# Kernel tuning notes

Hardware: AMD Instinct MI355X
Metric: run time of the kernel (lower is better)

Reference implementation:

```python
import jax, jax.numpy as jnp
import numpy as np
from jax import lax

B, N, CIN, MID, OUT, G, H, CHILDS = 16, 1024, 256, 512, 256, 4, 1, 512


def _ln(x, g, b, eps=1e-6):
    m = x.mean(-1, keepdims=True)
    v = ((x - m) ** 2).mean(-1, keepdims=True)
    return (x - m) / jnp.sqrt(v + eps) * g + b


def _gconv(x, W, b):
    # grouped 1x1 conv1d: x [B,Cin,N], W [Cout, Cin//G], b [Cout]
    Bb, Cin, Nn = x.shape
    Cout = W.shape[0]
    xg = x.reshape(Bb, G, Cin // G, Nn)
    Wg = W.reshape(G, Cout // G, Cin // G)
    y = jnp.einsum('bgcn,goc->bgon', xg, Wg).reshape(Bb, Cout, Nn)
    return y + b[None, :, None]


def _forward(x, masks_roi1, masks_roi2, score_mask, gt_feat,
             W_att, b_att, W1, b1, W2, b2, g1, beta1, g2, beta2, Wg, bg):
    dt = x.dtype
    # gt branch
    gts = jax.nn.relu(gt_feat @ Wg + bg)  # [B,N,OUT]

    mr1 = masks_roi1 * score_mask[:, None, :]
    mr2 = masks_roi2 * score_mask[:, None, :]

    # attention logits without materializing the [B,N,N,2C] concat:
    # ft[b,i,j] = cat(x[b,j], x[b,i]);  logits = ft @ W_att + b_att
    Wq, Wk = W_att[:CIN], W_att[CIN:]
    lj = jnp.einsum('bjc,ch->bjh', x, Wq)  # query part (varies over j)
    li = jnp.einsum('bic,ch->bih', x, Wk)  # key part   (varies over i)
    attn = jax.nn.sigmoid(lj[:, None, :, :] + li[:, :, None, :] + b_att)  # [B,N,N,H]

    attn1 = attn * mr1[:, :, :, None]
    attn2 = attn * mr2[:, :, :, None]

    # torch fancy-index assign atten_mask[:,:,idces,:]=1 reduces to: any column
    # index appearing in ANY topk index set gets 1 along dim 2 for all b,i,h.
    k4, k2 = CHILDS // 4, CHILDS // 2
    a1 = jnp.moveaxis(attn1, 2, 3)  # [B,N,H,N] -> topk over last axis (= dim 2)
    a2 = jnp.moveaxis(attn2, 2, 3)
    idx1 = lax.top_k(a1, k4)[1]
    idx1m = lax.top_k(-a1, k4)[1]
    idx2 = lax.top_k(a2, k2)[1]
    idx2m = lax.top_k(-a2, k4)[1]
    all_idx = jnp.concatenate([idx1.ravel(), idx1m.ravel(), idx2.ravel(), idx2m.ravel()])
    col = jnp.zeros((N,), dtype=dt).at[all_idx].set(1.0)

    attn = attn * (mr1 + mr2)[:, :, :, None] * col[None, None, :, None]

    f = (score_mask == 0).astype(dt)  # [B,N]
    f_diag = f[:, :, None] * jnp.eye(N, dtype=dt)  # diag_embed
    atten = (attn + f_diag[:, :, :, None]) / CHILDS
    atten = jnp.transpose(atten, (0, 3, 2, 1))  # [B,H,Nj,Ni]

    x_t = jnp.transpose(x, (0, 2, 1))  # [B,CIN,N]
    o1 = jax.nn.relu(_gconv(x_t, W1, b1))  # [B,MID,N]
    o1m = jnp.matmul(o1.reshape(B, H, MID // H, N), atten).reshape(B, MID, N)
    o1m = _ln(jnp.transpose(o1m, (0, 2, 1)), g1, beta1)  # [B,N,MID]
    o1 = o1 + jnp.transpose(o1m, (0, 2, 1))

    o2 = jax.nn.relu(_gconv(o1, W2, b2))  # [B,OUT,N]
    o2m = jnp.matmul(o2.reshape(B, H, OUT // H, N), atten).reshape(B, OUT, N)
    node_feat = _ln(jnp.transpose(o2m, (0, 2, 1)), g2, beta2)  # [B,N,OUT]
    o2 = o2 + jnp.transpose(node_feat, (0, 2, 1))
    output2 = jnp.transpose(o2, (0, 2, 1))  # [B,N,OUT]
    return output2, gts, node_feat


def setup_inputs() -> dict:
    key = jax.random.key(0)
    ks = jax.random.split(key, 16)
    x = jax.random.normal(ks[0], (B, N, CIN), jnp.float32)
    masks_roi1 = (jax.random.uniform(ks[1], (B, N, N)) < 0.1).astype(jnp.float32)
    masks_roi2 = (jax.random.uniform(ks[2], (B, N, N)) < 0.1).astype(jnp.float32)
    score_mask = (jax.random.uniform(ks[3], (B, N)) < 0.8).astype(jnp.float32)
    gt_feat = jax.random.normal(ks[4], (B, N, CIN), jnp.float32)
    s = 0.05
    W_att = jax.random.normal(ks[5], (2 * CIN, H), jnp.float32) * s
    b_att = jnp.zeros((H,), jnp.float32)
    W1 = jax.random.normal(ks[6], (MID, CIN // G), jnp.float32) * s
    b1 = jax.random.normal(ks[7], (MID,), jnp.float32) * s
    W2 = jax.random.normal(ks[8], (OUT, MID // G), jnp.float32) * s
    b2 = jax.random.normal(ks[9], (OUT,), jnp.float32) * s
    g1 = jax.random.normal(ks[10], (MID,), jnp.float32) * s
    beta1 = jnp.zeros((MID,), jnp.float32)
    g2 = jax.random.normal(ks[11], (OUT,), jnp.float32) * s
    beta2 = jnp.zeros((OUT,), jnp.float32)
    Wg = jax.random.normal(ks[12], (CIN, OUT), jnp.float32) * s
    bg = jax.random.normal(ks[13], (OUT,), jnp.float32) * s
    return {"x": x, "masks_roi1": masks_roi1, "masks_roi2": masks_roi2,
            "score_mask": score_mask, "gt_feat": gt_feat,
            "W_att": W_att, "b_att": b_att, "W1": W1, "b1": b1,
            "W2": W2, "b2": b2, "g1": g1, "beta1": beta1,
            "g2": g2, "beta2": beta2, "Wg": Wg, "bg": bg}


def reference(x, masks_roi1, masks_roi2, score_mask, gt_feat,
              W_att, b_att, W1, b1, W2, b2, g1, beta1, g2, beta2, Wg, bg):
    return _forward(x, masks_roi1, masks_roi2, score_mask, gt_feat,
                    W_att, b_att, W1, b1, W2, b2, g1, beta1, g2, beta2, Wg, bg)
```

## Files before the change

### kernel.cpp

```cpp
#include <hip/hip_runtime.h>
#include <cstddef>
#include <cstdint>

#define B_ 16
#define N_ 1024
#define CIN_ 256
#define MID_ 512
#define OUT_ 256

typedef __attribute__((ext_vector_type(8))) short short8v;
typedef __attribute__((ext_vector_type(4))) float f32x4;

__device__ __forceinline__ float sigf(float z){ return 1.f/(1.f+expf(-z)); }
__device__ __forceinline__ ushort f2bf(float f){
  uint32_t u=__float_as_uint(f);
  uint32_t r=(u + 0x7fffu + ((u>>16)&1u))>>16;
  return (ushort)r;
}
__device__ __forceinline__ float bf2f(ushort u){ return __uint_as_float(((uint32_t)u)<<16); }

__device__ __forceinline__ void async16(void* lds, const void* g){
  __builtin_amdgcn_global_load_lds(
      (const __attribute__((address_space(1))) uint32_t*)g,
      (__attribute__((address_space(3))) uint32_t*)lds,
      16, 0, 0);
}

__global__ __launch_bounds__(256) void k_prep(const float* __restrict__ x,
    const float* __restrict__ Watt, float* __restrict__ lj, float* __restrict__ li)
{
  int bn = blockIdx.x*256 + threadIdx.x;
  const float4* xr = (const float4*)(x + (size_t)bn*CIN_);
  const float4* wq = (const float4*)(Watt);
  const float4* wk = (const float4*)(Watt + CIN_);
  float aq=0.f, ak=0.f;
  #pragma unroll 8
  for(int c=0;c<CIN_/4;++c){
    float4 xv=xr[c]; float4 q=wq[c]; float4 w=wk[c];
    aq += xv.x*q.x+xv.y*q.y+xv.z*q.z+xv.w*q.w;
    ak += xv.x*w.x+xv.y*w.y+xv.z*w.z+xv.w*w.w;
  }
  lj[bn]=aq; li[bn]=ak;
}

__global__ __launch_bounds__(256) void k_cast(const float* __restrict__ s, ushort* __restrict__ d){
  int i = blockIdx.x*256 + threadIdx.x;
  float4 v = ((const float4*)s)[i];
  ((ushort4*)d)[i] = make_ushort4(f2bf(v.x), f2bf(v.y), f2bf(v.z), f2bf(v.w));
}
__global__ __launch_bounds__(256) void k_wgtb(const float* __restrict__ Wg, ushort* __restrict__ WgTb){
  int o=blockIdx.x, c=threadIdx.x;
  WgTb[(size_t)o*CIN_ + c] = f2bf(Wg[(size_t)c*OUT_ + o]);
}

__global__ __launch_bounds__(256) void k_col(
    const float* __restrict__ m1, const float* __restrict__ m2,
    const float* __restrict__ sc, const float* __restrict__ lj,
    const float* __restrict__ li, const float* __restrict__ batt,
    float* __restrict__ colf, ushort* __restrict__ mrs)
{
  int row = blockIdx.x; int b = row >> 10; int t = threadIdx.x;
  size_t base = (size_t)row*N_ + 4*t;
  float4 m1v = *(const float4*)(m1 + base);
  float4 m2v = *(const float4*)(m2 + base);
  float4 scv = *(const float4*)(sc + (b<<10) + 4*t);
  float mr1[4] = {m1v.x*scv.x, m1v.y*scv.y, m1v.z*scv.z, m1v.w*scv.w};
  float mr2[4] = {m2v.x*scv.x, m2v.y*scv.y, m2v.z*scv.z, m2v.w*scv.w};
  *(ushort4*)(mrs + base) = make_ushort4(f2bf(mr1[0]+mr2[0]), f2bf(mr1[1]+mr2[1]),
                                         f2bf(mr1[2]+mr2[2]), f2bf(mr1[3]+mr2[3]));
  int z1=0,z2=0;
  #pragma unroll
  for(int k=0;k<4;++k){ z1 += (mr1[k]==0.f); z2 += (mr2[k]==0.f); }
  __shared__ int sc1[256], sc2[256];
  __shared__ float A1s[1024], A2s[1024];
  sc1[t]=z1; sc2[t]=z2; __syncthreads();
  for(int off=1; off<256; off<<=1){
    int a=0,c=0;
    if(t>=off){ a=sc1[t-off]; c=sc2[t-off]; }
    __syncthreads();
    if(t>=off){ sc1[t]+=a; sc2[t]+=c; }
    __syncthreads();
  }
  int excl1 = sc1[t]-z1, excl2 = sc2[t]-z2;
  int Z1 = sc1[255], Z2 = sc2[255];
  int P1 = 1024-Z1, P2 = 1024-Z2;
  bool rare = (P1>128)||(P2>256)||(Z1<128)||(Z2<128);
  if(!rare){
    int zb1=excl1, zb2=excl2;
    #pragma unroll
    for(int k=0;k<4;++k){
      bool q = (mr1[k]!=0.f) || (zb1<128) || (mr2[k]!=0.f) || (zb2<128) || (P2+zb2<256);
      if(q) colf[4*t+k]=1.0f;
      zb1 += (mr1[k]==0.f); zb2 += (mr2[k]==0.f);
    }
  } else {
    float lir = li[row], ba = batt[0];
    float4 ljv = *(const float4*)(lj + (b<<10) + 4*t);
    float ljr[4]={ljv.x,ljv.y,ljv.z,ljv.w};
    #pragma unroll
    for(int k=0;k<4;++k){
      float v = sigf(ljr[k]+lir+ba);
      A1s[4*t+k]=mr1[k]*v; A2s[4*t+k]=mr2[k]*v;
    }
    __syncthreads();
    for(int k=0;k<4;++k){
      int j=4*t+k; float a1j=A1s[j], a2j=A2s[j];
      int r1=0,r1m=0,r2=0,r2m=0;
      for(int jp=0;jp<1024;++jp){
        float p1=A1s[jp], p2=A2s[jp];
        bool lo = jp<j;
        r1  += (p1>a1j)||((p1==a1j)&&lo);
        r1m += (p1<a1j)||((p1==a1j)&&lo);
        r2  += (p2>a2j)||((p2==a2j)&&lo);
        r2m += (p2<a2j)||((p2==a2j)&&lo);
      }
      if(r1<128||r1m<128||r2<256||r2m<128) colf[j]=1.0f;
    }
  }
}

__global__ __launch_bounds__(256) void k_at(const ushort* __restrict__ mrs,
    const float* __restrict__ sc, const float* __restrict__ lj,
    const float* __restrict__ li, const float* __restrict__ batt,
    const float* __restrict__ colf, ushort* __restrict__ Atb)
{
  int row=blockIdx.x, t=threadIdx.x; int b=row>>10, i=row&1023;
  size_t base=(size_t)row*N_ + 4*t;
  ushort4 mv=*(const ushort4*)(mrs+base);
  float4 ljv=*(const float4*)(lj + (b<<10) + 4*t);
  float4 cv =*(const float4*)(colf + 4*t);
  float lir=li[row], ba=batt[0];
  float fi = (sc[(b<<10)+i]==0.f)?1.f:0.f;
  float mra[4]={bf2f(mv.x),bf2f(mv.y),bf2f(mv.z),bf2f(mv.w)};
  float ljr[4]={ljv.x,ljv.y,ljv.z,ljv.w};
  float cr[4]={cv.x,cv.y,cv.z,cv.w};
  ushort o[4]; int j0=4*t;
  #pragma unroll
  for(int k=0;k<4;++k){
    float v=sigf(ljr[k]+lir+ba);
    float val=v*mra[k]*cr[k];
    if(j0+k==i) val+=fi;
    o[k]=f2bf(val*(1.f/512.f));
  }
  *(ushort4*)(Atb+base) = make_ushort4(o[0],o[1],o[2],o[3]);
}

__global__ __launch_bounds__(256) void mgemm(
    const ushort* __restrict__ A, int lda, long long sAb, long long sAg,
    const ushort* __restrict__ Bp, int ldb, long long sBb, long long sBg,
    float* __restrict__ C, ushort* __restrict__ Cb, int ldc, long long sCb, long long sCg,
    int K, int nG,
    const float* __restrict__ biasM, int biasMG,
    const float* __restrict__ biasN, int relu)
{
  __shared__ __align__(16) ushort As[128*32];
  __shared__ __align__(16) ushort Bs[128*32];
  int z=blockIdx.z, b=z/nG, g=z%nG;
  A  += b*sAb + g*sAg;
  Bp += b*sBb + g*sBg;
  size_t cOff = (size_t)b*sCb + (size_t)g*sCg;
  int m0 = blockIdx.y*128, n0 = blockIdx.x*128;
  int tid=threadIdx.x, w=tid>>6, lane=tid&63;
  int la=lane&15, hi=lane>>4;
  int wr=w>>1, wc=w&1;
  f32x4 acc[4][4] = {};
  int sr = tid>>2;
  int sk = (tid&3)*8;
  char* lA = (char*)As + w*1024;
  char* lB = (char*)Bs + w*1024;
  const ushort* gA0 = A + (size_t)(m0+sr)*lda + sk;
  const ushort* gA1 = A + (size_t)(m0+64+sr)*lda + sk;
  const ushort* gB0 = Bp + (size_t)(n0+sr)*ldb + sk;
  const ushort* gB1 = Bp + (size_t)(n0+64+sr)*ldb + sk;
  for(int k0=0;k0<K;k0+=32){
    async16(lA,        gA0 + k0);
    async16(lA + 4096, gA1 + k0);
    async16(lB,        gB0 + k0);
    async16(lB + 4096, gB1 + k0);
    __syncthreads();
    short8v af[4], bf[4];
    #pragma unroll
    for(int i2=0;i2<4;++i2) af[i2] = *(const short8v*)&As[(wr*64+i2*16+la)*32 + hi*8];
    #pragma unroll
    for(int j2=0;j2<4;++j2) bf[j2] = *(const short8v*)&Bs[(wc*64+j2*16+la)*32 + hi*8];
    #pragma unroll
    for(int i2=0;i2<4;++i2)
      #pragma unroll
      for(int j2=0;j2<4;++j2)
        acc[i2][j2] = __builtin_amdgcn_mfma_f32_16x16x32_bf16(af[i2], bf[j2], acc[i2][j2], 0,0,0);
    __syncthreads();
  }
  float* Cp = C + cOff;
  ushort* Cbp = Cb ? Cb + cOff : (ushort*)0;
  #pragma unroll
  for(int i2=0;i2<4;++i2){
    int row0 = m0 + wr*64 + i2*16 + hi*4;
    #pragma unroll
    for(int j2=0;j2<4;++j2){
      int col = n0 + wc*64 + j2*16 + la;
      float bn = biasN ? biasN[col] : 0.f;
      #pragma unroll
      for(int r=0;r<4;++r){
        int row = row0 + r;
        float v = acc[i2][j2][r] + bn + (biasM ? biasM[(size_t)g*biasMG + row] : 0.f);
        if(relu) v = fmaxf(v, 0.f);
        Cp[(size_t)row*ldc + col] = v;
        if(Cbp) Cbp[(size_t)row*ldc + col] = f2bf(v);
      }
    }
  }
}

template<int BM,int BN,int TM,int TN>
__global__ __launch_bounds__(256) void gemm_nt(
    const float* __restrict__ A, int lda, long long sAb, long long sAg,
    const float* __restrict__ Bp, int ldb, long long sBb, long long sBg,
    float* __restrict__ C, ushort* __restrict__ Cbd, int ldc, long long sCb, long long sCg,
    int K, int nG,
    const float* __restrict__ biasM, int biasMG,
    const float* __restrict__ biasN, int relu)
{
  static_assert(TN==4 && BM/TM==16 && BN/TN==16, "layout");
  constexpr int BK=32, LDSS=BK+4;
  int z=blockIdx.z, b=z/nG, g=z%nG;
  A  += b*sAb + g*sAg;
  Bp += b*sBb + g*sBg;
  size_t cOff = (size_t)b*sCb + (size_t)g*sCg;
  __shared__ float As[BM*LDSS];
  __shared__ float Bs[BN*LDSS];
  int tid=threadIdx.x;
  int tx=tid&15, ty=tid>>4;
  int m0=blockIdx.y*BM, n0=blockIdx.x*BN;
  float acc[TM][TN]={};
  for(int k0=0;k0<K;k0+=BK){
    #pragma unroll
    for(int u=0;u<BM*BK/1024;++u){
      int f=u*256+tid, r=f>>3, c=(f&7)*4;
      *(float4*)&As[r*LDSS+c] = *(const float4*)(A + (size_t)(m0+r)*lda + k0 + c);
    }
    #pragma unroll
    for(int u=0;u<BN*BK/1024;++u){
      int f=u*256+tid, r=f>>3, c=(f&7)*4;
      *(float4*)&Bs[r*LDSS+c] = *(const float4*)(Bp + (size_t)(n0+r)*ldb + k0 + c);
    }
    __syncthreads();
    #pragma unroll
    for(int kk=0;kk<BK;kk+=4){
      float4 av[TM]; float4 bv[TN];
      #pragma unroll
      for(int r=0;r<TM;++r) av[r]=*(const float4*)&As[(ty*TM+r)*LDSS+kk];
      #pragma unroll
      for(int c=0;c<TN;++c) bv[c]=*(const float4*)&Bs[(tx*TN+c)*LDSS+kk];
      #pragma unroll
      for(int r=0;r<TM;++r){
        #pragma unroll
        for(int c=0;c<TN;++c){
          acc[r][c] += av[r].x*bv[c].x + av[r].y*bv[c].y + av[r].z*bv[c].z + av[r].w*bv[c].w;
        }
      }
    }
    __syncthreads();
  }
  float4 bnv=make_float4(0.f,0.f,0.f,0.f);
  if(biasN){ bnv=*(const float4*)(biasN + n0 + tx*TN); }
  #pragma unroll
  for(int r=0;r<TM;++r){
    int m=m0+ty*TM+r;
    float bm = biasM ? biasM[(size_t)g*biasMG + m] : 0.f;
    float4 v;
    v.x=acc[r][0]+bm+bnv.x;
    v.y=acc[r][1]+bm+bnv.y;
    v.z=acc[r][2]+bm+bnv.z;
    v.w=acc[r][3]+bm+bnv.w;
    if(relu){ v.x=fmaxf(v.x,0.f); v.y=fmaxf(v.y,0.f); v.z=fmaxf(v.z,0.f); v.w=fmaxf(v.w,0.f); }
    *(float4*)(C + cOff + (size_t)m*ldc + n0 + tx*TN) = v;
    if(Cbd){
      *(ushort4*)(Cbd + cOff + (size_t)m*ldc + n0 + tx*TN) =
          make_ushort4(f2bf(v.x), f2bf(v.y), f2bf(v.z), f2bf(v.w));
    }
  }
}

__global__ __launch_bounds__(256) void k_ln1(const float* o1mT, const float* o1,
    const float* __restrict__ g1v, const float* __restrict__ be1, float* o1pT)
{
  int row=blockIdx.x, t=threadIdx.x; int b=row>>10, i=row&1023;
  float2 v = ((const float2*)(o1mT + (size_t)row*MID_))[t];
  float s=v.x+v.y, s2=v.x*v.x+v.y*v.y;
  for(int off=32; off; off>>=1){ s+=__shfl_down(s,off); s2+=__shfl_down(s2,off); }
  __shared__ float sm[8];
  int lane=t&63, wid=t>>6;
  if(lane==0){ sm[wid]=s; sm[4+wid]=s2; }
  __syncthreads();
  s=sm[0]+sm[1]+sm[2]+sm[3]; s2=sm[4]+sm[5]+sm[6]+sm[7];
  float mean=s*(1.f/MID_), var=s2*(1.f/MID_)-mean*mean;
  float rstd=rsqrtf(var+1e-6f);
  int m0=2*t;
  float a0=(v.x-mean)*rstd*g1v[m0]+be1[m0];
  float a1=(v.y-mean)*rstd*g1v[m0+1]+be1[m0+1];
  float2 o;
  o.x = a0 + o1[((size_t)(b*MID_+m0  ))*N_ + i];
  o.y = a1 + o1[((size_t)(b*MID_+m0+1))*N_ + i];
  ((float2*)(o1pT + (size_t)row*MID_))[t] = o;
}

__global__ __launch_bounds__(256) void k_ln2f(const float* o2mT, const float* o2,
    const float* __restrict__ g2v, const float* __restrict__ be2,
    float* node, float* out2)
{
  int row=blockIdx.x, t=threadIdx.x; int b=row>>10, i=row&1023;
  float v = o2mT[(size_t)row*OUT_ + t];
  float s=v, s2=v*v;
  for(int off=32; off; off>>=1){ s+=__shfl_down(s,off); s2+=__shfl_down(s2,off); }
  __shared__ float sm[8];
  int lane=t&63, wid=t>>6;
  if(lane==0){ sm[wid]=s; sm[4+wid]=s2; }
  __syncthreads();
  s=sm[0]+sm[1]+sm[2]+sm[3]; s2=sm[4]+sm[5]+sm[6]+sm[7];
  float mean=s*(1.f/OUT_); float var=s2*(1.f/OUT_)-mean*mean;
  float rstd=rsqrtf(var+1e-6f);
  float nf=(v-mean)*rstd*g2v[t]+be2[t];
  size_t ro=(size_t)row*OUT_+t;
  node[ro]=nf;
  out2[ro]=nf + o2[((size_t)(b*OUT_+t))*N_ + i];
}

extern "C" void kernel_launch(void* const* d_in, const int* in_sizes, int n_in,
                              void* d_out, int out_size, void* d_ws, size_t ws_size,
                              hipStream_t stream)
{
  const float* x    = (const float*)d_in[0];
  const float* m1   = (const float*)d_in[1];
  const float* m2   = (const float*)d_in[2];
  const float* sc   = (const float*)d_in[3];
  const float* gt   = (const float*)d_in[4];
  const float* Watt = (const float*)d_in[5];
  const float* batt = (const float*)d_in[6];
  const float* W1   = (const float*)d_in[7];
  const float* b1   = (const float*)d_in[8];
  const float* W2   = (const float*)d_in[9];
  const float* b2   = (const float*)d_in[10];
  const float* g1   = (const float*)d_in[11];
  const float* be1  = (const float*)d_in[12];
  const float* g2   = (const float*)d_in[13];
  const float* be2  = (const float*)d_in[14];
  const float* Wg   = (const float*)d_in[15];
  const float* bg   = (const float*)d_in[16];

  float* out2 = (float*)d_out;
  float* gtso = out2 + (size_t)B_*N_*OUT_;
  float* node = gtso + (size_t)B_*N_*OUT_;

  char* ws = (char*)d_ws;
  float*  colf = (float*)(ws);
  float*  lj   = (float*)(ws + 4096);
  float*  li   = (float*)(ws + 69632);
  ushort* WgTb = (ushort*)(ws + 135168);
  ushort* W1b  = (ushort*)(ws + 266240);
  ushort* gtb  = (ushort*)(ws + 331776);
  ushort* Atb  = (ushort*)(ws + 8720384);
  float*  o1   = (float*)(ws + 42274816);
  ushort* o1b  = (ushort*)(ws + 75829248);
  char*   big32 = ws + 92606464;
  ushort* mrs  = (ushort*)big32;
  ushort* xb   = (ushort*)big32;
  float*  o1mT = (float*)big32;
  float*  o1pT = o1mT;
  float*  o2   = o1;
  ushort* o2b  = o1b;
  float*  o2mT = o1mT;

  hipMemsetAsync(colf, 0, 4096, stream);
  k_prep<<<dim3(B_*N_/256),dim3(256),0,stream>>>(x,Watt,lj,li);
  k_col <<<dim3(B_*N_),dim3(256),0,stream>>>(m1,m2,sc,lj,li,batt,colf,mrs);
  k_at  <<<dim3(B_*N_),dim3(256),0,stream>>>(mrs,sc,lj,li,batt,colf,Atb);

  k_cast<<<dim3(4096),dim3(256),0,stream>>>(x, xb);
  k_cast<<<dim3(4096),dim3(256),0,stream>>>(gt, gtb);
  k_cast<<<dim3(32),dim3(256),0,stream>>>(W1, W1b);
  k_wgtb<<<dim3(OUT_),dim3(256),0,stream>>>(Wg, WgTb);

  mgemm<<<dim3(2,128,1),256,0,stream>>>(
      gtb, CIN_, 0,0,
      WgTb, CIN_, 0,0,
      gtso, (ushort*)0, OUT_, 0,0,
      CIN_, 1, nullptr,0, bg, 1);

  mgemm<<<dim3(8,1,B_*4),256,0,stream>>>(
      W1b, 64, 0, (long long)128*64,
      xb, CIN_, (long long)N_*CIN_, 64,
      o1, o1b, N_, (long long)MID_*N_, (long long)128*N_,
      64, 4, b1, 128, nullptr, 1);

  mgemm<<<dim3(4,8,B_),256,0,stream>>>(
      Atb, N_, (long long)N_*N_, 0,
      o1b, N_, (long long)MID_*N_, 0,
      o1mT, (ushort*)0, MID_, (long long)N_*MID_, 0,
      N_, 1, nullptr,0, nullptr, 0);

  k_ln1<<<dim3(B_*N_),256,0,stream>>>(o1mT, o1, g1, be1, o1pT);

  gemm_nt<64,64,4,4><<<dim3(N_/64, 1, B_*4),256,0,stream>>>(
      W2, 128, 0, (long long)64*128,
      o1pT, MID_, (long long)N_*MID_, 128,
      o2, o2b, N_, (long long)OUT_*N_, (long long)64*N_,
      128, 4, b2, 64, nullptr, 1);

  mgemm<<<dim3(2,8,B_),256,0,stream>>>(
      Atb, N_, (long long)N_*N_, 0,
      o2b, N_, (long long)OUT_*N_, 0,
      o2mT, (ushort*)0, OUT_, (long long)N_*OUT_, 0,
      N_, 1, nullptr,0, nullptr, 0);

  k_ln2f<<<dim3(B_*N_),256,0,stream>>>(o2mT, o2, g2, be2, node, out2);
}
```

Baseline: 468.3 us.

## Move W2 GEMM to bf16 MFMA, drop fp32 intermediates, warp-per-row k_col

Replaces the fp32 SIMT gemm_nt for the W2 grouped conv with a templated bf16 MFMA GEMM, and stops writing fp32 copies of o1/o2 by reading residuals from the bf16 buffers. It also merges the cast kernels into fewer launches and rewrites k_col to process one row per wavefront using shuffle scans instead of block-level LDS scans. The rare fallback path now recomputes values from global memory instead of using shared memory. Residual adds now use bf16-rounded values, which adds precision risk.

```diff
diff --git a/kernel.cpp b/kernel.cpp
--- a/kernel.cpp
+++ b/kernel.cpp
@@ -43,14 +43,23 @@
   lj[bn]=aq; li[bn]=ak;
 }
 
-__global__ __launch_bounds__(256) void k_cast(const float* __restrict__ s, ushort* __restrict__ d){
+__global__ __launch_bounds__(256) void k_cast2(const float* __restrict__ x,
+    const float* __restrict__ gt, ushort* __restrict__ xb, ushort* __restrict__ gtb)
+{
   int i = blockIdx.x*256 + threadIdx.x;
-  float4 v = ((const float4*)s)[i];
-  ((ushort4*)d)[i] = make_ushort4(f2bf(v.x), f2bf(v.y), f2bf(v.z), f2bf(v.w));
-}
-__global__ __launch_bounds__(256) void k_wgtb(const float* __restrict__ Wg, ushort* __restrict__ WgTb){
-  int o=blockIdx.x, c=threadIdx.x;
-  WgTb[(size_t)o*CIN_ + c] = f2bf(Wg[(size_t)c*OUT_ + o]);
+  int which = i>>20; int idx = i & 1048575;
+  float4 v = ((const float4*)(which ? gt : x))[idx];
+  ((ushort4*)(which ? gtb : xb))[idx] = make_ushort4(f2bf(v.x), f2bf(v.y), f2bf(v.z), f2bf(v.w));
+}
+
+__global__ __launch_bounds__(256) void k_wcast(const float* __restrict__ W1,
+    const float* __restrict__ W2, const float* __restrict__ Wg,
+    ushort* __restrict__ W1b, ushort* __restrict__ W2b, ushort* __restrict__ WgTb)
+{
+  int bid=blockIdx.x, t=threadIdx.x;
+  if(bid<128){ int i=bid*256+t; W1b[i]=f2bf(W1[i]); }
+  else if(bid<256){ int i=(bid-128)*256+t; W2b[i]=f2bf(W2[i]); }
+  else { int idx=(bid-256)*256+t; int o=idx>>8, c=idx&255; WgTb[idx]=f2bf(Wg[(size_t)c*OUT_+o]); }
 }
 
 __global__ __launch_bounds__(256) void k_col(
@@ -59,62 +68,71 @@
     const float* __restrict__ li, const float* __restrict__ batt,
     float* __restrict__ colf, ushort* __restrict__ mrs)
 {
-  int row = blockIdx.x; int b = row >> 10; int t = threadIdx.x;
-  size_t base = (size_t)row*N_ + 4*t;
-  float4 m1v = *(const float4*)(m1 + base);
-  float4 m2v = *(const float4*)(m2 + base);
-  float4 scv = *(const float4*)(sc + (b<<10) + 4*t);
-  float mr1[4] = {m1v.x*scv.x, m1v.y*scv.y, m1v.z*scv.z, m1v.w*scv.w};
-  float mr2[4] = {m2v.x*scv.x, m2v.y*scv.y, m2v.z*scv.z, m2v.w*scv.w};
-  *(ushort4*)(mrs + base) = make_ushort4(f2bf(mr1[0]+mr2[0]), f2bf(mr1[1]+mr2[1]),
-                                         f2bf(mr1[2]+mr2[2]), f2bf(mr1[3]+mr2[3]));
-  int z1=0,z2=0;
-  #pragma unroll
-  for(int k=0;k<4;++k){ z1 += (mr1[k]==0.f); z2 += (mr2[k]==0.f); }
-  __shared__ int sc1[256], sc2[256];
-  __shared__ float A1s[1024], A2s[1024];
-  sc1[t]=z1; sc2[t]=z2; __syncthreads();
-  for(int off=1; off<256; off<<=1){
-    int a=0,c=0;
-    if(t>=off){ a=sc1[t-off]; c=sc2[t-off]; }
-    __syncthreads();
-    if(t>=off){ sc1[t]+=a; sc2[t]+=c; }
-    __syncthreads();
-  }
-  int excl1 = sc1[t]-z1, excl2 = sc2[t]-z2;
-  int Z1 = sc1[255], Z2 = sc2[255];
-  int P1 = 1024-Z1, P2 = 1024-Z2;
+  int wid = threadIdx.x>>6, lane = threadIdx.x&63;
+  int row = blockIdx.x*4 + wid; int b = row>>10;
+  size_t base = (size_t)row*N_ + lane*16;
+  const float4* m1p = (const float4*)(m1+base);
+  const float4* m2p = (const float4*)(m2+base);
+  const float4* scp = (const float4*)(sc + (b<<10) + lane*16);
+  float mr1[16], mr2[16];
+  int z1=0, z2=0;
+  #pragma unroll
+  for(int q=0;q<4;++q){
+    float4 a=m1p[q], c=m2p[q], s=scp[q];
+    mr1[4*q+0]=a.x*s.x; mr1[4*q+1]=a.y*s.y; mr1[4*q+2]=a.z*s.z; mr1[4*q+3]=a.w*s.w;
+    mr2[4*q+0]=c.x*s.x; mr2[4*q+1]=c.y*s.y; mr2[4*q+2]=c.z*s.z; mr2[4*q+3]=c.w*s.w;
+    #pragma unroll
+    for(int k=0;k<4;++k){ z1 += (mr1[4*q+k]==0.f); z2 += (mr2[4*q+k]==0.f); }
+  }
+  ushort mb[16];
+  #pragma unroll
+  for(int k=0;k<16;++k) mb[k]=f2bf(mr1[k]+mr2[k]);
+  *(short8v*)(mrs+base)   = *(short8v*)&mb[0];
+  *(short8v*)(mrs+base+8) = *(short8v*)&mb[8];
+  int s1=z1, s2=z2;
+  #pragma unroll
+  for(int off=1; off<64; off<<=1){
+    int t1=__shfl_up(s1,off), t2=__shfl_up(s2,off);
+    if(lane>=off){ s1+=t1; s2+=t2; }
+  }
+  int excl1=s1-z1, excl2=s2-z2;
+  int Z1=__shfl(s1,63), Z2=__shfl(s2,63);
+  int P1=1024-Z1, P2=1024-Z2;
   bool rare = (P1>128)||(P2>256)||(Z1<128)||(Z2<128);
   if(!rare){
     int zb1=excl1, zb2=excl2;
     #pragma unroll
-    for(int k=0;k<4;++k){
+    for(int k=0;k<16;++k){
       bool q = (mr1[k]!=0.f) || (zb1<128) || (mr2[k]!=0.f) || (zb2<128) || (P2+zb2<256);
-      if(q) colf[4*t+k]=1.0f;
+      if(q) colf[lane*16+k]=1.0f;
       zb1 += (mr1[k]==0.f); zb2 += (mr2[k]==0.f);
     }
   } else {
-    float lir = li[row], ba = batt[0];
-    float4 ljv = *(const float4*)(lj + (b<<10) + 4*t);
-    float ljr[4]={ljv.x,ljv.y,ljv.z,ljv.w};
-    #pragma unroll
-    for(int k=0;k<4;++k){
-      float v = sigf(ljr[k]+lir+ba);
-      A1s[4*t+k]=mr1[k]*v; A2s[4*t+k]=mr2[k]*v;
-    }
-    __syncthreads();
-    for(int k=0;k<4;++k){
-      int j=4*t+k; float a1j=A1s[j], a2j=A2s[j];
-      int r1=0,r1m=0,r2=0,r2m=0;
-      for(int jp=0;jp<1024;++jp){
-        float p1=A1s[jp], p2=A2s[jp];
+    float lir=li[row], ba=batt[0];
+    const float* m1r = m1 + (size_t)row*N_;
+    const float* m2r = m2 + (size_t)row*N_;
+    const float* scr = sc + (b<<10);
+    const float* ljr = lj + (b<<10);
+    float a1v[16], a2v[16];
+    #pragma unroll
+    for(int k=0;k<16;++k){
+      float v = sigf(ljr[lane*16+k]+lir+ba);
+      a1v[k]=mr1[k]*v; a2v[k]=mr2[k]*v;
+    }
+    for(int k=0;k<16;++k){
+      int j = lane*16+k;
+      int c1=0,c1m=0,c2=0,c2m=0;
+      for(int jp=0;jp<N_;++jp){
+        float sv=scr[jp];
+        float vv=sigf(ljr[jp]+lir+ba);
+        float p1=m1r[jp]*sv*vv, p2=m2r[jp]*sv*vv;
         bool lo = jp<j;
-        r1  += (p1>a1j)||((p1==a1j)&&lo);
-        r1m += (p1<a1j)||((p1==a1j)&&lo);
-        r2  += (p2>a2j)||((p2==a2j)&&lo);
-        r2m += (p2<a2j)||((p2==a2j)&&lo);
+        c1 += (p1>a1v[k])||((p1==a1v[k])&&lo);
+        c1m+= (p1<a1v[k])||((p1==a1v[k])&&lo);
+        c2 += (p2>a2v[k])||((p2==a2v[k])&&lo);
+        c2m+= (p2<a2v[k])||((p2==a2v[k])&&lo);
       }
-      if(r1<128||r1m<128||r2<256||r2m<128) colf[j]=1.0f;
+      if(c1<128||c1m<128||c2<256||c2m<128) colf[j]=1.0f;
     }
   }
 }
@@ -145,6 +163,7 @@
   *(ushort4*)(Atb+base) = make_ushort4(o[0],o[1],o[2],o[3]);
 }
 
+template<int BM,int BN,int WR,int WC>
 __global__ __launch_bounds__(256) void mgemm(
     const ushort* __restrict__ A, int lda, long long sAb, long long sAg,
     const ushort* __restrict__ Bp, int ldb, long long sBb, long long sBg,
@@ -153,45 +172,46 @@
     const float* __restrict__ biasM, int biasMG,
     const float* __restrict__ biasN, int relu)
 {
-  __shared__ __align__(16) ushort As[128*32];
-  __shared__ __align__(16) ushort Bs[128*32];
+  static_assert(WR*WC==4 && BM==WR*64 && BN==WC*64, "tile");
+  __shared__ __align__(16) ushort As[BM*32];
+  __shared__ __align__(16) ushort Bs[BN*32];
   int z=blockIdx.z, b=z/nG, g=z%nG;
-  A  += b*sAb + g*sAg;
-  Bp += b*sBb + g*sBg;
+  A  += (size_t)b*sAb + (size_t)g*sAg;
+  Bp += (size_t)b*sBb + (size_t)g*sBg;
   size_t cOff = (size_t)b*sCb + (size_t)g*sCg;
-  int m0 = blockIdx.y*128, n0 = blockIdx.x*128;
+  int m0 = blockIdx.y*BM, n0 = blockIdx.x*BN;
   int tid=threadIdx.x, w=tid>>6, lane=tid&63;
   int la=lane&15, hi=lane>>4;
-  int wr=w>>1, wc=w&1;
+  int wr=w/WC, wc=w%WC;
   f32x4 acc[4][4] = {};
-  int sr = tid>>2;
-  int sk = (tid&3)*8;
-  char* lA = (char*)As + w*1024;
-  char* lB = (char*)Bs + w*1024;
-  const ushort* gA0 = A + (size_t)(m0+sr)*lda + sk;
-  const ushort* gA1 = A + (size_t)(m0+64+sr)*lda + sk;
-  const ushort* gB0 = Bp + (size_t)(n0+sr)*ldb + sk;
-  const ushort* gB1 = Bp + (size_t)(n0+64+sr)*ldb + sk;
+  constexpr int RND = (BM+BN)/64;
+  int srow = lane>>2;
+  int sk8  = (lane&3)*8;
   for(int k0=0;k0<K;k0+=32){
-    async16(lA,        gA0 + k0);
-    async16(lA + 4096, gA1 + k0);
-    async16(lB,        gB0 + k0);
-    async16(lB + 4096, gB1 + k0);
+    #pragma unroll
+    for(int r=0;r<RND;++r){
+      int row0 = r*64 + w*16;
+      if(row0 < BM){
+        const ushort* src = A + (size_t)(m0+row0+srow)*lda + k0 + sk8;
+        async16((char*)As + row0*64, src);
+      } else {
+        const ushort* src = Bp + (size_t)(n0+row0-BM+srow)*ldb + k0 + sk8;
+        async16((char*)Bs + (row0-BM)*64, src);
+      }
+    }
     __syncthreads();
-    short8v af[4], bf[4];
+    short8v af[4], bf4[4];
     #pragma unroll
     for(int i2=0;i2<4;++i2) af[i2] = *(const short8v*)&As[(wr*64+i2*16+la)*32 + hi*8];
     #pragma unroll
-    for(int j2=0;j2<4;++j2) bf[j2] = *(const short8v*)&Bs[(wc*64+j2*16+la)*32 + hi*8];
+    for(int j2=0;j2<4;++j2) bf4[j2] = *(const short8v*)&Bs[(wc*64+j2*16+la)*32 + hi*8];
     #pragma unroll
     for(int i2=0;i2<4;++i2)
       #pragma unroll
       for(int j2=0;j2<4;++j2)
-        acc[i2][j2] = __builtin_amdgcn_mfma_f32_16x16x32_bf16(af[i2], bf[j2], acc[i2][j2], 0,0,0);
+        acc[i2][j2] = __builtin_amdgcn_mfma_f32_16x16x32_bf16(af[i2], bf4[j2], acc[i2][j2], 0,0,0);
     __syncthreads();
   }
-  float* Cp = C + cOff;
-  ushort* Cbp = Cb ? Cb + cOff : (ushort*)0;
   #pragma unroll
   for(int i2=0;i2<4;++i2){
     int row0 = m0 + wr*64 + i2*16 + hi*4;
@@ -204,85 +224,16 @@
         int row = row0 + r;
         float v = acc[i2][j2][r] + bn + (biasM ? biasM[(size_t)g*biasMG + row] : 0.f);
         if(relu) v = fmaxf(v, 0.f);
-        Cp[(size_t)row*ldc + col] = v;
-        if(Cbp) Cbp[(size_t)row*ldc + col] = f2bf(v);
+        if(C)  C [cOff + (size_t)row*ldc + col] = v;
+        if(Cb) Cb[cOff + (size_t)row*ldc + col] = f2bf(v);
       }
     }
   }
 }
 
-template<int BM,int BN,int TM,int TN>
-__global__ __launch_bounds__(256) void gemm_nt(
-    const float* __restrict__ A, int lda, long long sAb, long long sAg,
-    const float* __restrict__ Bp, int ldb, long long sBb, long long sBg,
-    float* __restrict__ C, ushort* __restrict__ Cbd, int ldc, long long sCb, long long sCg,
-    int K, int nG,
-    const float* __restrict__ biasM, int biasMG,
-    const float* __restrict__ biasN, int relu)
-{
-  static_assert(TN==4 && BM/TM==16 && BN/TN==16, "layout");
-  constexpr int BK=32, LDSS=BK+4;
-  int z=blockIdx.z, b=z/nG, g=z%nG;
-  A  += b*sAb + g*sAg;
-  Bp += b*sBb + g*sBg;
-  size_t cOff = (size_t)b*sCb + (size_t)g*sCg;
-  __shared__ float As[BM*LDSS];
-  __shared__ float Bs[BN*LDSS];
-  int tid=threadIdx.x;
-  int tx=tid&15, ty=tid>>4;
-  int m0=blockIdx.y*BM, n0=blockIdx.x*BN;
-  float acc[TM][TN]={};
-  for(int k0=0;k0<K;k0+=BK){
-    #pragma unroll
-    for(int u=0;u<BM*BK/1024;++u){
-      int f=u*256+tid, r=f>>3, c=(f&7)*4;
-      *(float4*)&As[r*LDSS+c] = *(const float4*)(A + (size_t)(m0+r)*lda + k0 + c);
-    }
-    #pragma unroll
-    for(int u=0;u<BN*BK/1024;++u){
-      int f=u*256+tid, r=f>>3, c=(f&7)*4;
-      *(float4*)&Bs[r*LDSS+c] = *(const float4*)(Bp + (size_t)(n0+r)*ldb + k0 + c);
-    }
-    __syncthreads();
-    #pragma unroll
-    for(int kk=0;kk<BK;kk+=4){
-      float4 av[TM]; float4 bv[TN];
-      #pragma unroll
-      for(int r=0;r<TM;++r) av[r]=*(const float4*)&As[(ty*TM+r)*LDSS+kk];
-      #pragma unroll
-      for(int c=0;c<TN;++c) bv[c]=*(const float4*)&Bs[(tx*TN+c)*LDSS+kk];
-      #pragma unroll
-      for(int r=0;r<TM;++r){
-        #pragma unroll
-        for(int c=0;c<TN;++c){
-          acc[r][c] += av[r].x*bv[c].x + av[r].y*bv[c].y + av[r].z*bv[c].z + av[r].w*bv[c].w;
-        }
-      }
-    }
-    __syncthreads();
-  }
-  float4 bnv=make_float4(0.f,0.f,0.f,0.f);
-  if(biasN){ bnv=*(const float4*)(biasN + n0 + tx*TN); }
-  #pragma unroll
-  for(int r=0;r<TM;++r){
-    int m=m0+ty*TM+r;
-    float bm = biasM ? biasM[(size_t)g*biasMG + m] : 0.f;
-    float4 v;
-    v.x=acc[r][0]+bm+bnv.x;
-    v.y=acc[r][1]+bm+bnv.y;
-    v.z=acc[r][2]+bm+bnv.z;
-    v.w=acc[r][3]+bm+bnv.w;
-    if(relu){ v.x=fmaxf(v.x,0.f); v.y=fmaxf(v.y,0.f); v.z=fmaxf(v.z,0.f); v.w=fmaxf(v.w,0.f); }
-    *(float4*)(C + cOff + (size_t)m*ldc + n0 + tx*TN) = v;
-    if(Cbd){
-      *(ushort4*)(Cbd + cOff + (size_t)m*ldc + n0 + tx*TN) =
-          make_ushort4(f2bf(v.x), f2bf(v.y), f2bf(v.z), f2bf(v.w));
-    }
-  }
-}
-
-__global__ __launch_bounds__(256) void k_ln1(const float* o1mT, const float* o1,
-    const float* __restrict__ g1v, const float* __restrict__ be1, float* o1pT)
+__global__ __launch_bounds__(256) void k_ln1(const float* __restrict__ o1mT,
+    const ushort* __restrict__ o1b,
+    const float* __restrict__ g1v, const float* __restrict__ be1, ushort* __restrict__ o1pb)
 {
   int row=blockIdx.x, t=threadIdx.x; int b=row>>10, i=row&1023;
   float2 v = ((const float2*)(o1mT + (size_t)row*MID_))[t];
@@ -298,15 +249,16 @@
   int m0=2*t;
   float a0=(v.x-mean)*rstd*g1v[m0]+be1[m0];
   float a1=(v.y-mean)*rstd*g1v[m0+1]+be1[m0+1];
-  float2 o;
-  o.x = a0 + o1[((size_t)(b*MID_+m0  ))*N_ + i];
-  o.y = a1 + o1[((size_t)(b*MID_+m0+1))*N_ + i];
-  ((float2*)(o1pT + (size_t)row*MID_))[t] = o;
-}
-
-__global__ __launch_bounds__(256) void k_ln2f(const float* o2mT, const float* o2,
+  float r0 = bf2f(o1b[((size_t)(b*MID_+m0  ))*N_ + i]);
+  float r1 = bf2f(o1b[((size_t)(b*MID_+m0+1))*N_ + i]);
+  ushort2 o; o.x=f2bf(a0+r0); o.y=f2bf(a1+r1);
+  ((ushort2*)(o1pb + (size_t)row*MID_))[t] = o;
+}
+
+__global__ __launch_bounds__(256) void k_ln2f(const float* __restrict__ o2mT,
+    const ushort* __restrict__ o2b,
     const float* __restrict__ g2v, const float* __restrict__ be2,
-    float* node, float* out2)
+    float* __restrict__ node, float* __restrict__ out2)
 {
   int row=blockIdx.x, t=threadIdx.x; int b=row>>10, i=row&1023;
   float v = o2mT[(size_t)row*OUT_ + t];
@@ -322,7 +274,7 @@
   float nf=(v-mean)*rstd*g2v[t]+be2[t];
   size_t ro=(size_t)row*OUT_+t;
   node[ro]=nf;
-  out2[ro]=nf + o2[((size_t)(b*OUT_+t))*N_ + i];
+  out2[ro]=nf + bf2f(o2b[((size_t)(b*OUT_+t))*N_ + i]);
 }
 
 extern "C" void kernel_launch(void* const* d_in, const int* in_sizes, int n_in,
@@ -355,62 +307,60 @@
   float*  colf = (float*)(ws);
   float*  lj   = (float*)(ws + 4096);
   float*  li   = (float*)(ws + 69632);
-  ushort* WgTb = (ushort*)(ws + 135168);
-  ushort* W1b  = (ushort*)(ws + 266240);
-  ushort* gtb  = (ushort*)(ws + 331776);
-  ushort* Atb  = (ushort*)(ws + 8720384);
-  float*  o1   = (float*)(ws + 42274816);
-  ushort* o1b  = (ushort*)(ws + 75829248);
-  char*   big32 = ws + 92606464;
-  ushort* mrs  = (ushort*)big32;
-  ushort* xb   = (ushort*)big32;
-  float*  o1mT = (float*)big32;
-  float*  o1pT = o1mT;
-  float*  o2   = o1;
-  ushort* o2b  = o1b;
-  float*  o2mT = o1mT;
+  ushort* W1b  = (ushort*)(ws + 135168);
+  ushort* W2b  = (ushort*)(ws + 200704);
+  ushort* WgTb = (ushort*)(ws + 266240);
+  char* R1 = ws + 1048576;
+  ushort* mrs  = (ushort*)R1;
+  float*  o1mT = (float*)R1;
+  ushort* Atb  = (ushort*)(ws + 34603008);
+  char* R3 = ws + 68157440;
+  ushort* xb  = (ushort*)R3;
+  ushort* gtb = (ushort*)(R3 + 8388608);
+  ushort* o2b = (ushort*)R3;
+  ushort* o1b = (ushort*)(ws + 84934656);
+  char* R5 = ws + 101711872;
+  ushort* o1pb = (ushort*)R5;
+  float*  o2mT = (float*)R5;
 
   hipMemsetAsync(colf, 0, 4096, stream);
-  k_prep<<<dim3(B_*N_/256),dim3(256),0,stream>>>(x,Watt,lj,li);
-  k_col <<<dim3(B_*N_),dim3(256),0,stream>>>(m1,m2,sc,lj,li,batt,colf,mrs);
-  k_at  <<<dim3(B_*N_),dim3(256),0,stream>>>(mrs,sc,lj,li,batt,colf,Atb);
-
-  k_cast<<<dim3(4096),dim3(256),0,stream>>>(x, xb);
-  k_cast<<<dim3(4096),dim3(256),0,stream>>>(gt, gtb);
-  k_cast<<<dim3(32),dim3(256),0,stream>>>(W1, W1b);
-  k_wgtb<<<dim3(OUT_),dim3(256),0,stream>>>(Wg, WgTb);
-
-  mgemm<<<dim3(2,128,1),256,0,stream>>>(
+  k_prep <<<dim3(B_*N_/256),dim3(256),0,stream>>>(x,Watt,lj,li);
+  k_cast2<<<dim3(8192),dim3(256),0,stream>>>(x, gt, xb, gtb);
+  k_wcast<<<dim3(512),dim3(256),0,stream>>>(W1, W2, Wg, W1b, W2b, WgTb);
+  k_col  <<<dim3(B_*N_/4),dim3(256),0,stream>>>(m1,m2,sc,lj,li,batt,colf,mrs);
+  k_at   <<<dim3(B_*N_),dim3(256),0,stream>>>(mrs,sc,lj,li,batt,colf,Atb);
+
+  mgemm<128,128,2,2><<<dim3(2,128,1),256,0,stream>>>(
       gtb, CIN_, 0,0,
       WgTb, CIN_, 0,0,
       gtso, (ushort*)0, OUT_, 0,0,
       CIN_, 1, nullptr,0, bg, 1);
 
-  mgemm<<<dim3(8,1,B_*4),256,0,stream>>>(
+  mgemm<128,128,2,2><<<dim3(8,1,B_*4),256,0,stream>>>(
       W1b, 64, 0, (long long)128*64,
       xb, CIN_, (long long)N_*CIN_, 64,
-      o1, o1b, N_, (long long)MID_*N_, (long long)128*N_,
+      (float*)0, o1b, N_, (long long)MID_*N_, (long long)128*N_,
       64, 4, b1, 128, nullptr, 1);
 
-  mgemm<<<dim3(4,8,B_),256,0,stream>>>(
+  mgemm<128,128,2,2><<<dim3(4,8,B_),256,0,stream>>>(
       Atb, N_, (long long)N_*N_, 0,
       o1b, N_, (long long)MID_*N_, 0,
       o1mT, (ushort*)0, MID_, (long long)N_*MID_, 0,
       N_, 1, nullptr,0, nullptr, 0);
 
-  k_ln1<<<dim3(B_*N_),256,0,stream>>>(o1mT, o1, g1, be1, o1pT);
-
-  gemm_nt<64,64,4,4><<<dim3(N_/64, 1, B_*4),256,0,stream>>>(
-      W2, 128, 0, (long long)64*128,
-      o1pT, MID_, (long long)N_*MID_, 128,
-      o2, o2b, N_, (long long)OUT_*N_, (long long)64*N_,
+  k_ln1<<<dim3(B_*N_),256,0,stream>>>(o1mT, o1b, g1, be1, o1pb);
+
+  mgemm<64,256,1,4><<<dim3(4,1,B_*4),256,0,stream>>>(
+      W2b, 128, 0, (long long)64*128,
+      o1pb, MID_, (long long)N_*MID_, 128,
+      (float*)0, o2b, N_, (long long)OUT_*N_, (long long)64*N_,
       128, 4, b2, 64, nullptr, 1);
 
-  mgemm<<<dim3(2,8,B_),256,0,stream>>>(
+  mgemm<128,128,2,2><<<dim3(2,8,B_),256,0,stream>>>(
       Atb, N_, (long long)N_*N_, 0,
       o2b, N_, (long long)OUT_*N_, 0,
       o2mT, (ushort*)0, OUT_, (long long)N_*OUT_, 0,
       N_, 1, nullptr,0, nullptr, 0);
 
-  k_ln2f<<<dim3(B_*N_),256,0,stream>>>(o2mT, o2, g2, be2, node, out2);
-}
+  k_ln2f<<<dim3(B_*N_),256,0,stream>>>(o2mT, o2b, g2, be2, node, out2);
+}
```

New measurement: 465.2 us. No clear change (-0.7%).
